# Optimization experiments

Measured on AMD Instinct MI355X. Metric: run time of the kernel, lower is better.

The kernel has to match this reference:

```python
import jax, jax.numpy as jnp
import numpy as np

N_HEAD = 8


def setup_inputs() -> dict:
    key = jax.random.key(0)
    ks = jax.random.split(key, 4)
    B, L, C = 4, 1024, 512
    x = jax.random.normal(ks[0], (B, L, C), dtype=jnp.float32)
    adj = jax.random.uniform(ks[1], (B, L, L), dtype=jnp.float32)
    W_qkv = jax.random.normal(ks[2], (3 * C, C), dtype=jnp.float32) * 0.02
    W_proj = jax.random.normal(ks[3], (C, C), dtype=jnp.float32) * 0.02
    bias_scale = jnp.array([3.0, 3.0], dtype=jnp.float32)
    beta = jnp.ones((3,), dtype=jnp.float32) / 3.0
    return {"x": x, "adj": adj, "W_qkv": W_qkv, "W_proj": W_proj,
            "bias_scale": bias_scale, "beta": beta}


def _branch_attn(Q, K, V, scale, bias=None):
    # Q,K,V: [B,H,L,D]
    S = jnp.einsum('bhqd,bhkd->bhqk', Q, K) / scale
    if bias is not None:
        S = S + bias
    attn = jax.nn.softmax(S, axis=-1)
    return jnp.einsum('bhqk,bhkd->bhqd', attn, V)


def reference(x, adj, W_qkv, W_proj, bias_scale, beta):
    B, L, C = x.shape
    H = N_HEAD
    D = C // H
    scale = jnp.sqrt(jnp.float32(D))

    qkv = x @ W_qkv.T  # [B,L,3C]
    Q, K, V = jnp.split(qkv, 3, axis=-1)
    Q = Q.reshape(B, L, H, D).transpose(0, 2, 1, 3)  # [B,H,L,D]
    K = K.reshape(B, L, H, D).transpose(0, 2, 1, 3)
    V = V.reshape(B, L, H, D).transpose(0, 2, 1, 3)

    # has_cls: zero out CLS row/col in adjacency
    adj_local = adj.at[:, 0, :].set(0.0).at[:, :, 0].set(0.0)
    B_fwd = adj_local[:, None, :, :]              # [B,1,L,L]
    B_bwd = jnp.swapaxes(adj_local, -1, -2)[:, None, :, :]

    h0 = _branch_attn(Q, K, V, scale)
    h1 = _branch_attn(Q, K, V, scale, bias_scale[0] * B_fwd)
    h2 = _branch_attn(Q, K, V, scale, bias_scale[1] * B_bwd)

    b = jax.nn.softmax(beta, axis=0)
    out = b[0] * h0 + b[1] * h1 + b[2] * h2      # [B,H,L,D]
    out = out.transpose(0, 2, 1, 3).reshape(B, L, C)
    return out @ W_proj.T
```

## Files before the change

### kernel.cpp

```cpp
#include <hip/hip_runtime.h>
#include <hip/hip_bf16.h>
#include <stdint.h>

#define B_  4
#define L_  1024
#define C_  512
#define H_  8
#define D_  64
#define BH_ 32
#define M_  4096

typedef short  bf16x8 __attribute__((ext_vector_type(8)));
typedef float  f32x4  __attribute__((ext_vector_type(4)));
typedef unsigned short u16x8 __attribute__((ext_vector_type(8)));
typedef unsigned int   u32x2 __attribute__((ext_vector_type(2)));

__device__ __forceinline__ unsigned short f2bf(float f) {
    union { float f; uint32_t u; } v; v.f = f;
    uint32_t u = v.u;
    return (unsigned short)((u + 0x7fffu + ((u >> 16) & 1u)) >> 16);
}
__device__ __forceinline__ float bf2f(unsigned short s) {
    union { uint32_t u; float f; } v; v.u = ((uint32_t)s) << 16;
    return v.f;
}

__device__ __forceinline__ void gload16(const void* g, void* s) {
    __builtin_amdgcn_global_load_lds((const __attribute__((address_space(1))) void*)g,
                                     (__attribute__((address_space(3))) void*)s, 16, 0, 0);
}

#define NX4   (M_ * C_ / 4)
#define NWQ4  (3 * C_ * C_ / 4)
#define NWP4  (C_ * C_ / 4)
__global__ void cvt_all(const float* __restrict__ x, const float* __restrict__ wq,
                        const float* __restrict__ wp,
                        unsigned short* __restrict__ xb, unsigned short* __restrict__ wqb,
                        unsigned short* __restrict__ wpb) {
    int i = blockIdx.x * 256 + threadIdx.x;
    const float* src; unsigned short* dst; int o;
    if (i < NX4) { src = x; dst = xb; o = i; }
    else if (i < NX4 + NWQ4) { src = wq; dst = wqb; o = i - NX4; }
    else if (i < NX4 + NWQ4 + NWP4) { src = wp; dst = wpb; o = i - NX4 - NWQ4; }
    else return;
    float4 v = ((const float4*)src)[o];
    ushort4 r;
    r.x = f2bf(v.x); r.y = f2bf(v.y); r.z = f2bf(v.z); r.w = f2bf(v.w);
    ((ushort4*)dst)[o] = r;
}

__global__ __launch_bounds__(256) void prep_e(const float* __restrict__ adj,
                                              const float* __restrict__ bias_scale,
                                              unsigned short* __restrict__ EI) {
    __shared__ float Tr[64][65];
    const int b = blockIdx.z, q0 = blockIdx.y * 64, k0 = blockIdx.x * 64;
    const float* adjb = adj + (size_t)b * L_ * L_;
    const int tid = threadIdx.x;
#pragma unroll
    for (int i = 0; i < 4; ++i) {
        int idx = i * 256 + tid;
        int rk = idx >> 4, c4 = (idx & 15) * 4;
        float4 v = *(const float4*)(adjb + (size_t)(k0 + rk) * L_ + q0 + c4);
        Tr[rk][c4 + 0] = v.x; Tr[rk][c4 + 1] = v.y; Tr[rk][c4 + 2] = v.z; Tr[rk][c4 + 3] = v.w;
    }
    __syncthreads();
    const float bs0 = bias_scale[0], bs1 = bias_scale[1];
    const int w = tid >> 6, l = tid & 63, g = l >> 4, c = l & 15;
#pragma unroll
    for (int qs = 0; qs < 4; ++qs) {
        int ql = qs * 16 + c, qg = q0 + ql;
        int klb = w * 16 + g * 4;
        float4 af4 = *(const float4*)(adjb + (size_t)qg * L_ + k0 + klb);
        unsigned short ef[4], eb[4];
        const float afv[4] = {af4.x, af4.y, af4.z, af4.w};
#pragma unroll
        for (int i = 0; i < 4; ++i) {
            int kg = k0 + klb + i;
            bool z = (qg == 0) || (kg == 0);
            ef[i] = f2bf(z ? 1.0f : __expf(bs0 * afv[i]));
            eb[i] = f2bf(z ? 1.0f : __expf(bs1 * Tr[klb + i][ql]));
        }
        size_t o = (((size_t)b * 64 + (blockIdx.y * 4 + qs)) * 64 + (blockIdx.x * 4 + w)) * 512 + (size_t)l * 8;
        u16x8 o8 = {ef[0], ef[1], ef[2], ef[3], eb[0], eb[1], eb[2], eb[3]};
        *(u16x8*)(EI + o) = o8;
    }
}

template <int BM, int BN, int KDIM, int EPI, int NDIM>
__global__ __launch_bounds__(256, 4) void gemm_bf16(const unsigned short* __restrict__ Amat,
                                                    const unsigned short* __restrict__ Bmat,
                                                    float* __restrict__ outp,
                                                    unsigned short* __restrict__ q_out,
                                                    unsigned short* __restrict__ k_out,
                                                    unsigned short* __restrict__ v_out) {
    constexpr int NA = BM / 32, NB = BN / 32;
    constexpr int MI = BM / 32, NI = BN / 32;
    __shared__ __align__(16) unsigned short As[BM * 64];
    __shared__ __align__(16) unsigned short Bs[BN * 64];
    const int tid = threadIdx.x;
    const int l = tid & 63, wid = tid >> 6;
    const int g = l >> 4, c = l & 15;
    const int wr = wid >> 1, wc = wid & 1;
    const int row0 = blockIdx.y * BM, col0 = blockIdx.x * BN;

    f32x4 acc[MI][NI];
#pragma unroll
    for (int mi = 0; mi < MI; ++mi)
#pragma unroll
        for (int ni = 0; ni < NI; ++ni) acc[mi][ni] = (f32x4){0.f, 0.f, 0.f, 0.f};

    for (int k0 = 0; k0 < KDIM; k0 += 64) {
        bf16x8 ra[NA], rb[NB];
#pragma unroll
        for (int i = 0; i < NA; ++i) {
            int q = i * 256 + tid;
            int r = q >> 3, cb = (q & 7) * 16;
            ra[i] = *(const bf16x8*)((const char*)Amat + (size_t)(row0 + r) * (KDIM * 2) + k0 * 2 + cb);
        }
#pragma unroll
        for (int i = 0; i < NB; ++i) {
            int q = i * 256 + tid;
            int r = q >> 3, cb = (q & 7) * 16;
            rb[i] = *(const bf16x8*)((const char*)Bmat + (size_t)(col0 + r) * (KDIM * 2) + k0 * 2 + cb);
        }
        __syncthreads();
#pragma unroll
        for (int i = 0; i < NA; ++i) {
            int q = i * 256 + tid;
            int r = q >> 3, cb = (q & 7) * 16;
            *(bf16x8*)((char*)As + r * 128 + (cb ^ ((r & 7) << 4))) = ra[i];
        }
#pragma unroll
        for (int i = 0; i < NB; ++i) {
            int q = i * 256 + tid;
            int r = q >> 3, cb = (q & 7) * 16;
            *(bf16x8*)((char*)Bs + r * 128 + (cb ^ ((r & 7) << 4))) = rb[i];
        }
        __syncthreads();
#pragma unroll
        for (int kk = 0; kk < 2; ++kk) {
            bf16x8 afr[MI], bfr[NI];
#pragma unroll
            for (int mi = 0; mi < MI; ++mi) {
                int r = wr * (BM / 2) + mi * 16 + c;
                afr[mi] = *(const bf16x8*)((const char*)As + r * 128 + ((kk * 64 + g * 16) ^ ((r & 7) << 4)));
            }
#pragma unroll
            for (int ni = 0; ni < NI; ++ni) {
                int r = wc * (BN / 2) + ni * 16 + c;
                bfr[ni] = *(const bf16x8*)((const char*)Bs + r * 128 + ((kk * 64 + g * 16) ^ ((r & 7) << 4)));
            }
#pragma unroll
            for (int mi = 0; mi < MI; ++mi)
#pragma unroll
                for (int ni = 0; ni < NI; ++ni)
                    acc[mi][ni] = __builtin_amdgcn_mfma_f32_16x16x32_bf16(afr[mi], bfr[ni], acc[mi][ni], 0, 0, 0);
        }
    }
#pragma unroll
    for (int mi = 0; mi < MI; ++mi) {
#pragma unroll
        for (int ni = 0; ni < NI; ++ni) {
#pragma unroll
            for (int ii = 0; ii < 4; ++ii) {
                int m = row0 + wr * (BM / 2) + mi * 16 + g * 4 + ii;
                int n = col0 + wc * (BN / 2) + ni * 16 + c;
                float val = acc[mi][ni][ii];
                if (EPI == 0) {
                    unsigned short v = f2bf(val);
                    int b = m >> 10, ll = m & 1023;
                    int which = n >> 9, cc = n & 511;
                    int hh = cc >> 6, d = cc & 63;
                    int bh = b * 8 + hh;
                    if (which == 0)      q_out[((size_t)bh * L_ + ll) * D_ + d] = v;
                    else if (which == 1) k_out[((size_t)bh * L_ + ll) * D_ + d] = v;
                    else                 v_out[((size_t)bh * D_ + d) * L_ + ll] = v;
                } else {
                    outp[(size_t)m * NDIM + n] = val;
                }
            }
        }
    }
}

struct EReg { bf16x8 e[4]; };

__global__ __launch_bounds__(256, 2) void attn_kernel(const unsigned short* __restrict__ Qb,
                                                      const unsigned short* __restrict__ Kb,
                                                      const unsigned short* __restrict__ Vtb,
                                                      const unsigned short* __restrict__ EI,
                                                      const float* __restrict__ beta,
                                                      unsigned short* __restrict__ hb) {
    __shared__ __align__(16) char smem[2][16384];
    const int tid = threadIdx.x;
    const int w = tid >> 6, l = tid & 63;
    const int g = l >> 4, c = l & 15;

    const int p = blockIdx.x;
    const int s = (p & 7) + 8 * (p >> 6);
    const int h = (p >> 3) & 7;
    const int b = s >> 4, qb = s & 15;
    const int bh = b * 8 + h;
    const int q0 = qb * 64 + w * 16;
    const int qt = qb * 4 + w;

    const unsigned short* Qrow = Qb + ((size_t)bh * L_ + q0 + c) * D_;
    const bf16x8 qf0 = *(const bf16x8*)(Qrow + g * 8);
    const bf16x8 qf1 = *(const bf16x8*)(Qrow + 32 + g * 8);

    const unsigned short* Kbase = Kb + (size_t)bh * L_ * D_;
    const unsigned short* Vbase = Vtb + (size_t)bh * D_ * L_;
    const unsigned short* Ebase = EI + ((size_t)(b * 64 + qt) * 64) * 512;

    f32x4 O[3][4];
#pragma unroll
    for (int j = 0; j < 3; ++j)
#pragma unroll
        for (int dc = 0; dc < 4; ++dc) O[j][dc] = (f32x4){0.f, 0.f, 0.f, 0.f};
    float lsum0 = 0.f, lsum1 = 0.f, lsum2 = 0.f;

    const int srow = l >> 3, sm = l & 7;
    const int key = (c & 7) << 4;

    auto stage = [&](int t, char* base) {
#pragma unroll
        for (int n = 0; n < 2; ++n) {
            int i = 2 * w + n;
            int row = i * 8 + srow;
            int sw = (sm ^ (row & 7)) * 8;
            gload16(Kbase + (size_t)(t * 64 + row) * D_ + sw, base + i * 1024);
            gload16(Vbase + (size_t)row * L_ + t * 64 + sw, base + 8192 + i * 1024);
        }
    };
    auto eload = [&](EReg& X, int t) {
#pragma unroll
        for (int ks = 0; ks < 4; ++ks)
            X.e[ks] = *(const bf16x8*)(Ebase + (size_t)(t * 4 + ks) * 512 + l * 8);
    };

    auto compute = [&](const char* base, const EReg& E) {
        const char* Kl = base;
        const char* Vl = base + 8192;
        unsigned r[4][3][2];
#pragma unroll
        for (int st = 0; st < 4; ++st) {
            const char* kr = Kl + (st * 16 + c) * 128;
            bf16x8 ka = *(const bf16x8*)(kr + ((g * 16) ^ key));
            bf16x8 kb = *(const bf16x8*)(kr + ((64 + g * 16) ^ key));
            f32x4 sacc = (f32x4){0.f, 0.f, 0.f, 0.f};
            sacc = __builtin_amdgcn_mfma_f32_16x16x32_bf16(ka, qf0, sacc, 0, 0, 0);
            sacc = __builtin_amdgcn_mfma_f32_16x16x32_bf16(kb, qf1, sacc, 0, 0, 0);
            float pv[3][4];
#pragma unroll
            for (int i = 0; i < 4; ++i) {
                float p0 = __expf(sacc[i] * 0.125f);
                float p1 = p0 * bf2f((unsigned short)E.e[st][i]);
                float p2 = p0 * bf2f((unsigned short)E.e[st][4 + i]);
                lsum0 += p0; lsum1 += p1; lsum2 += p2;
                pv[0][i] = p0; pv[1][i] = p1; pv[2][i] = p2;
            }
#pragma unroll
            for (int j = 0; j < 3; ++j) {
                r[st][j][0] = __builtin_amdgcn_perm(__float_as_uint(pv[j][1]), __float_as_uint(pv[j][0]), 0x07060302u);
                r[st][j][1] = __builtin_amdgcn_perm(__float_as_uint(pv[j][3]), __float_as_uint(pv[j][2]), 0x07060302u);
            }
        }
#pragma unroll
        for (int kk = 0; kk < 2; ++kk) {
            bf16x8 af[3];
#pragma unroll
            for (int j = 0; j < 3; ++j) {
                union { unsigned u[4]; bf16x8 v; } t_;
                t_.u[0] = r[2 * kk][j][0];     t_.u[1] = r[2 * kk][j][1];
                t_.u[2] = r[2 * kk + 1][j][0]; t_.u[3] = r[2 * kk + 1][j][1];
                af[j] = t_.v;
            }
#pragma unroll
            for (int dc = 0; dc < 4; ++dc) {
                const char* vr = Vl + (dc * 16 + c) * 128;
                u32x2 vlo = *(const u32x2*)(vr + ((kk * 64 + g * 8) ^ key));
                u32x2 vhi = *(const u32x2*)(vr + ((kk * 64 + 32 + g * 8) ^ key));
                union { unsigned u[4]; bf16x8 v; } bv;
                bv.u[0] = vlo[0]; bv.u[1] = vlo[1]; bv.u[2] = vhi[0]; bv.u[3] = vhi[1];
#pragma unroll
                for (int j = 0; j < 3; ++j)
                    O[j][dc] = __builtin_amdgcn_mfma_f32_16x16x32_bf16(af[j], bv.v, O[j][dc], 0, 0, 0);
            }
        }
    };

    EReg E0, E1;
    stage(0, smem[0]);
    eload(E0, 0);
    __syncthreads();
#pragma unroll 1
    for (int t = 0; t < 16; t += 2) {
        stage(t + 1, smem[1]);
        eload(E1, t + 1);
        compute(smem[0], E0);
        __syncthreads();
        if (t + 2 < 16) { stage(t + 2, smem[0]); eload(E0, t + 2); }
        compute(smem[1], E1);
        __syncthreads();
    }

    lsum0 += __shfl_xor(lsum0, 16); lsum0 += __shfl_xor(lsum0, 32);
    lsum1 += __shfl_xor(lsum1, 16); lsum1 += __shfl_xor(lsum1, 32);
    lsum2 += __shfl_xor(lsum2, 16); lsum2 += __shfl_xor(lsum2, 32);

    float b0 = beta[0], b1 = beta[1], b2 = beta[2];
    float bm = fmaxf(b0, fmaxf(b1, b2));
    float e0 = __expf(b0 - bm), e1 = __expf(b1 - bm), e2 = __expf(b2 - bm);
    float inv = 1.0f / (e0 + e1 + e2);
    float i0 = e0 * inv / lsum0, i1 = e1 * inv / lsum1, i2 = e2 * inv / lsum2;

    float iq0[4], iq1[4], iq2[4];
#pragma unroll
    for (int ii = 0; ii < 4; ++ii) {
        iq0[ii] = __shfl(i0, g * 4 + ii);
        iq1[ii] = __shfl(i1, g * 4 + ii);
        iq2[ii] = __shfl(i2, g * 4 + ii);
    }
    const int hcol = (bh & 7) * 64;
#pragma unroll
    for (int dc = 0; dc < 4; ++dc) {
#pragma unroll
        for (int ii = 0; ii < 4; ++ii) {
            float hv = iq0[ii] * O[0][dc][ii] + iq1[ii] * O[1][dc][ii] + iq2[ii] * O[2][dc][ii];
            int qrow = q0 + g * 4 + ii;
            hb[((size_t)(b << 10) + qrow) * C_ + hcol + dc * 16 + c] = f2bf(hv);
        }
    }
}

extern "C" void kernel_launch(void* const* d_in, const int* in_sizes, int n_in,
                              void* d_out, int out_size, void* d_ws, size_t ws_size,
                              hipStream_t stream) {
    const float* x          = (const float*)d_in[0];
    const float* adj        = (const float*)d_in[1];
    const float* wqkv       = (const float*)d_in[2];
    const float* wproj      = (const float*)d_in[3];
    const float* bias_scale = (const float*)d_in[4];
    const float* beta       = (const float*)d_in[5];
    float* out = (float*)d_out;

    char* ws = (char*)d_ws;
    size_t off = 0;
    auto alloc = [&](size_t bytes) {
        void* p = ws + off;
        off += (bytes + 255) & ~(size_t)255;
        return p;
    };
    unsigned short* xb     = (unsigned short*)alloc((size_t)M_ * C_ * 2);
    unsigned short* wqkvb  = (unsigned short*)alloc((size_t)3 * C_ * C_ * 2);
    unsigned short* wprojb = (unsigned short*)alloc((size_t)C_ * C_ * 2);
    unsigned short* Qb     = (unsigned short*)alloc((size_t)BH_ * L_ * D_ * 2);
    unsigned short* Kb     = (unsigned short*)alloc((size_t)BH_ * L_ * D_ * 2);
    unsigned short* Vtb    = (unsigned short*)alloc((size_t)BH_ * D_ * L_ * 2);
    unsigned short* EI     = (unsigned short*)alloc((size_t)B_ * L_ * L_ * 4);
    unsigned short* hb     = (unsigned short*)alloc((size_t)M_ * C_ * 2);

    cvt_all<<<(NX4 + NWQ4 + NWP4 + 255) / 256, 256, 0, stream>>>(x, wqkv, wproj, xb, wqkvb, wprojb);
    prep_e<<<dim3(L_ / 64, L_ / 64, B_), 256, 0, stream>>>(adj, bias_scale, EI);
    gemm_bf16<64, 128, 512, 0, 0><<<dim3(1536 / 128, M_ / 64), 256, 0, stream>>>(xb, wqkvb, nullptr, Qb, Kb, Vtb);
    attn_kernel<<<dim3(512), 256, 0, stream>>>(Qb, Kb, Vtb, EI, beta, hb);
    gemm_bf16<64, 64, 512, 1, 512><<<dim3(512 / 64, M_ / 64), 256, 0, stream>>>(hb, wprojb, out, nullptr, nullptr, nullptr);
}
```

Before: 71.84 us.

## Fuse x conversion into QKV GEMM, symmetric adj tiles, deepen attention pipeline

Removes the separate fp32-to-bf16 conversion of x by converting it inside the QKV GEMM's A-operand load. prep_e now processes tile pairs (i,j) and (j,i) together, so each adjacency tile is read once instead of twice. The attention kernel moves from a two-buffer to a four-buffer LDS pipeline, with explicit vmcnt waits, raw barriers, and S/PV compute split so loads overlap compute further ahead. The four buffers double LDS use to 64KB, which could reduce occupancy, and half of the prep_e blocks now exit immediately.

```diff
diff --git a/kernel.cpp b/kernel.cpp
--- a/kernel.cpp
+++ b/kernel.cpp
@@ -5,7 +5,6 @@
 #define B_  4
 #define L_  1024
 #define C_  512
-#define H_  8
 #define D_  64
 #define BH_ 32
 #define M_  4096
@@ -30,18 +29,14 @@
                                      (__attribute__((address_space(3))) void*)s, 16, 0, 0);
 }
 
-#define NX4   (M_ * C_ / 4)
 #define NWQ4  (3 * C_ * C_ / 4)
 #define NWP4  (C_ * C_ / 4)
-__global__ void cvt_all(const float* __restrict__ x, const float* __restrict__ wq,
-                        const float* __restrict__ wp,
-                        unsigned short* __restrict__ xb, unsigned short* __restrict__ wqb,
-                        unsigned short* __restrict__ wpb) {
+__global__ void cvt_w(const float* __restrict__ wq, const float* __restrict__ wp,
+                      unsigned short* __restrict__ wqb, unsigned short* __restrict__ wpb) {
     int i = blockIdx.x * 256 + threadIdx.x;
     const float* src; unsigned short* dst; int o;
-    if (i < NX4) { src = x; dst = xb; o = i; }
-    else if (i < NX4 + NWQ4) { src = wq; dst = wqb; o = i - NX4; }
-    else if (i < NX4 + NWQ4 + NWP4) { src = wp; dst = wpb; o = i - NX4 - NWQ4; }
+    if (i < NWQ4) { src = wq; dst = wqb; o = i; }
+    else if (i < NWQ4 + NWP4) { src = wp; dst = wpb; o = i - NWQ4; }
     else return;
     float4 v = ((const float4*)src)[o];
     ushort4 r;
@@ -52,42 +47,59 @@
 __global__ __launch_bounds__(256) void prep_e(const float* __restrict__ adj,
                                               const float* __restrict__ bias_scale,
                                               unsigned short* __restrict__ EI) {
-    __shared__ float Tr[64][65];
-    const int b = blockIdx.z, q0 = blockIdx.y * 64, k0 = blockIdx.x * 64;
-    const float* adjb = adj + (size_t)b * L_ * L_;
+    const int bI = blockIdx.z;
+    const int i = blockIdx.y, j = blockIdx.x;
+    if (j < i) return;
+    __shared__ float Ta[64][68];
+    __shared__ float Tb[64][68];
+    const float* adjb = adj + (size_t)bI * L_ * L_;
     const int tid = threadIdx.x;
 #pragma unroll
-    for (int i = 0; i < 4; ++i) {
-        int idx = i * 256 + tid;
-        int rk = idx >> 4, c4 = (idx & 15) * 4;
-        float4 v = *(const float4*)(adjb + (size_t)(k0 + rk) * L_ + q0 + c4);
-        Tr[rk][c4 + 0] = v.x; Tr[rk][c4 + 1] = v.y; Tr[rk][c4 + 2] = v.z; Tr[rk][c4 + 3] = v.w;
+    for (int s = 0; s < 4; ++s) {
+        int idx = s * 256 + tid;
+        int r = idx >> 4, c4 = (idx & 15) * 4;
+        float4 va = *(const float4*)(adjb + (size_t)(i * 64 + r) * L_ + j * 64 + c4);
+        float4 vb = *(const float4*)(adjb + (size_t)(j * 64 + r) * L_ + i * 64 + c4);
+        *(float4*)&Ta[r][c4] = va;
+        *(float4*)&Tb[r][c4] = vb;
     }
     __syncthreads();
     const float bs0 = bias_scale[0], bs1 = bias_scale[1];
     const int w = tid >> 6, l = tid & 63, g = l >> 4, c = l & 15;
+    const int kloc = w * 16 + g * 4;
 #pragma unroll
     for (int qs = 0; qs < 4; ++qs) {
-        int ql = qs * 16 + c, qg = q0 + ql;
-        int klb = w * 16 + g * 4;
-        float4 af4 = *(const float4*)(adjb + (size_t)qg * L_ + k0 + klb);
-        unsigned short ef[4], eb[4];
-        const float afv[4] = {af4.x, af4.y, af4.z, af4.w};
-#pragma unroll
-        for (int i = 0; i < 4; ++i) {
-            int kg = k0 + klb + i;
-            bool z = (qg == 0) || (kg == 0);
-            ef[i] = f2bf(z ? 1.0f : __expf(bs0 * afv[i]));
-            eb[i] = f2bf(z ? 1.0f : __expf(bs1 * Tr[klb + i][ql]));
-        }
-        size_t o = (((size_t)b * 64 + (blockIdx.y * 4 + qs)) * 64 + (blockIdx.x * 4 + w)) * 512 + (size_t)l * 8;
-        u16x8 o8 = {ef[0], ef[1], ef[2], ef[3], eb[0], eb[1], eb[2], eb[3]};
-        *(u16x8*)(EI + o) = o8;
-    }
-}
-
-template <int BM, int BN, int KDIM, int EPI, int NDIM>
+        const int qloc = qs * 16 + c;
+        {
+            int qg = i * 64 + qloc, kgb = j * 64 + kloc;
+            unsigned short ef[4], eb[4];
+#pragma unroll
+            for (int e = 0; e < 4; ++e) {
+                bool z = (qg == 0) || (kgb + e == 0);
+                ef[e] = f2bf(z ? 1.0f : __expf(bs0 * Ta[qloc][kloc + e]));
+                eb[e] = f2bf(z ? 1.0f : __expf(bs1 * Tb[kloc + e][qloc]));
+            }
+            size_t o = (((size_t)bI * 64 + (i * 4 + qs)) * 64 + (j * 4 + w)) * 512 + (size_t)l * 8;
+            *(u16x8*)(EI + o) = (u16x8){ef[0], ef[1], ef[2], ef[3], eb[0], eb[1], eb[2], eb[3]};
+        }
+        if (i != j) {
+            int qg = j * 64 + qloc, kgb = i * 64 + kloc;
+            unsigned short ef[4], eb[4];
+#pragma unroll
+            for (int e = 0; e < 4; ++e) {
+                bool z = (qg == 0) || (kgb + e == 0);
+                ef[e] = f2bf(z ? 1.0f : __expf(bs0 * Tb[qloc][kloc + e]));
+                eb[e] = f2bf(z ? 1.0f : __expf(bs1 * Ta[kloc + e][qloc]));
+            }
+            size_t o = (((size_t)bI * 64 + (j * 4 + qs)) * 64 + (i * 4 + w)) * 512 + (size_t)l * 8;
+            *(u16x8*)(EI + o) = (u16x8){ef[0], ef[1], ef[2], ef[3], eb[0], eb[1], eb[2], eb[3]};
+        }
+    }
+}
+
+template <int BM, int BN, int KDIM, int EPI, int NDIM, bool AF32>
 __global__ __launch_bounds__(256, 4) void gemm_bf16(const unsigned short* __restrict__ Amat,
+                                                    const float* __restrict__ Af,
                                                     const unsigned short* __restrict__ Bmat,
                                                     float* __restrict__ outp,
                                                     unsigned short* __restrict__ q_out,
@@ -114,8 +126,18 @@
 #pragma unroll
         for (int i = 0; i < NA; ++i) {
             int q = i * 256 + tid;
-            int r = q >> 3, cb = (q & 7) * 16;
-            ra[i] = *(const bf16x8*)((const char*)Amat + (size_t)(row0 + r) * (KDIM * 2) + k0 * 2 + cb);
+            int r = q >> 3;
+            if constexpr (AF32) {
+                const float* ap = Af + (size_t)(row0 + r) * KDIM + k0 + (q & 7) * 8;
+                float4 v0 = *(const float4*)ap;
+                float4 v1 = *(const float4*)(ap + 4);
+                union { unsigned short s[8]; bf16x8 v; } u;
+                u.s[0] = f2bf(v0.x); u.s[1] = f2bf(v0.y); u.s[2] = f2bf(v0.z); u.s[3] = f2bf(v0.w);
+                u.s[4] = f2bf(v1.x); u.s[5] = f2bf(v1.y); u.s[6] = f2bf(v1.z); u.s[7] = f2bf(v1.w);
+                ra[i] = u.v;
+            } else {
+                ra[i] = *(const bf16x8*)((const char*)Amat + (size_t)(row0 + r) * (KDIM * 2) + k0 * 2 + (q & 7) * 16);
+            }
         }
 #pragma unroll
         for (int i = 0; i < NB; ++i) {
@@ -191,7 +213,7 @@
                                                       const unsigned short* __restrict__ EI,
                                                       const float* __restrict__ beta,
                                                       unsigned short* __restrict__ hb) {
-    __shared__ __align__(16) char smem[2][16384];
+    __shared__ __align__(16) char smem[4][16384];
     const int tid = threadIdx.x;
     const int w = tid >> 6, l = tid & 63;
     const int g = l >> 4, c = l & 15;
@@ -207,6 +229,7 @@
     const unsigned short* Qrow = Qb + ((size_t)bh * L_ + q0 + c) * D_;
     const bf16x8 qf0 = *(const bf16x8*)(Qrow + g * 8);
     const bf16x8 qf1 = *(const bf16x8*)(Qrow + 32 + g * 8);
+    asm volatile("s_waitcnt vmcnt(0)" ::: "memory");
 
     const unsigned short* Kbase = Kb + (size_t)bh * L_ * D_;
     const unsigned short* Vbase = Vtb + (size_t)bh * D_ * L_;
@@ -238,10 +261,8 @@
             X.e[ks] = *(const bf16x8*)(Ebase + (size_t)(t * 4 + ks) * 512 + l * 8);
     };
 
-    auto compute = [&](const char* base, const EReg& E) {
+    auto computeS = [&](const char* base, const EReg& E, unsigned (&rr)[4][3][2]) {
         const char* Kl = base;
-        const char* Vl = base + 8192;
-        unsigned r[4][3][2];
 #pragma unroll
         for (int st = 0; st < 4; ++st) {
             const char* kr = Kl + (st * 16 + c) * 128;
@@ -261,18 +282,22 @@
             }
 #pragma unroll
             for (int j = 0; j < 3; ++j) {
-                r[st][j][0] = __builtin_amdgcn_perm(__float_as_uint(pv[j][1]), __float_as_uint(pv[j][0]), 0x07060302u);
-                r[st][j][1] = __builtin_amdgcn_perm(__float_as_uint(pv[j][3]), __float_as_uint(pv[j][2]), 0x07060302u);
-            }
-        }
+                rr[st][j][0] = __builtin_amdgcn_perm(__float_as_uint(pv[j][1]), __float_as_uint(pv[j][0]), 0x07060302u);
+                rr[st][j][1] = __builtin_amdgcn_perm(__float_as_uint(pv[j][3]), __float_as_uint(pv[j][2]), 0x07060302u);
+            }
+        }
+    };
+
+    auto computePV = [&](const char* base, const unsigned (&rr)[4][3][2]) {
+        const char* Vl = base + 8192;
 #pragma unroll
         for (int kk = 0; kk < 2; ++kk) {
             bf16x8 af[3];
 #pragma unroll
             for (int j = 0; j < 3; ++j) {
                 union { unsigned u[4]; bf16x8 v; } t_;
-                t_.u[0] = r[2 * kk][j][0];     t_.u[1] = r[2 * kk][j][1];
-                t_.u[2] = r[2 * kk + 1][j][0]; t_.u[3] = r[2 * kk + 1][j][1];
+                t_.u[0] = rr[2 * kk][j][0];     t_.u[1] = rr[2 * kk][j][1];
+                t_.u[2] = rr[2 * kk + 1][j][0]; t_.u[3] = rr[2 * kk + 1][j][1];
                 af[j] = t_.v;
             }
 #pragma unroll
@@ -289,20 +314,46 @@
         }
     };
 
-    EReg E0, E1;
-    stage(0, smem[0]);
-    eload(E0, 0);
-    __syncthreads();
+    EReg EA, EB;
+    stage(0, smem[0]);  asm volatile("" ::: "memory");
+    eload(EA, 0);       asm volatile("" ::: "memory");
+    stage(1, smem[1]);  asm volatile("" ::: "memory");
+    eload(EB, 1);       asm volatile("" ::: "memory");
+
+#define PH_FULL(kk, EX, STT, VMS)                                          \
+    {                                                                      \
+        asm volatile("s_waitcnt vmcnt(" VMS ")" ::: "memory");             \
+        __builtin_amdgcn_s_barrier();                                      \
+        __builtin_amdgcn_sched_barrier(0);                                 \
+        unsigned rr[4][3][2];                                              \
+        stage(STT, smem[(kk + 2) & 3]);  asm volatile("" ::: "memory");    \
+        computeS(smem[kk], EX, rr);                                        \
+        eload(EX, STT);                  asm volatile("" ::: "memory");    \
+        computePV(smem[kk], rr);                                           \
+    }
+#define PH_TAIL(kk, EX, VMS)                                               \
+    {                                                                      \
+        asm volatile("s_waitcnt vmcnt(" VMS ")" ::: "memory");             \
+        __builtin_amdgcn_s_barrier();                                      \
+        __builtin_amdgcn_sched_barrier(0);                                 \
+        unsigned rr[4][3][2];                                              \
+        computeS(smem[kk], EX, rr);                                        \
+        computePV(smem[kk], rr);                                           \
+    }
+
 #pragma unroll 1
-    for (int t = 0; t < 16; t += 2) {
-        stage(t + 1, smem[1]);
-        eload(E1, t + 1);
-        compute(smem[0], E0);
-        __syncthreads();
-        if (t + 2 < 16) { stage(t + 2, smem[0]); eload(E0, t + 2); }
-        compute(smem[1], E1);
-        __syncthreads();
-    }
+    for (int t = 0; t < 12; t += 4) {
+        PH_FULL(0, EA, t + 2, "12")
+        PH_FULL(1, EB, t + 3, "12")
+        PH_FULL(2, EA, t + 4, "12")
+        PH_FULL(3, EB, t + 5, "12")
+    }
+    PH_FULL(0, EA, 14, "12")
+    PH_FULL(1, EB, 15, "12")
+    PH_TAIL(2, EA, "12")
+    PH_TAIL(3, EB, "4")
+#undef PH_FULL
+#undef PH_TAIL
 
     lsum0 += __shfl_xor(lsum0, 16); lsum0 += __shfl_xor(lsum0, 32);
     lsum1 += __shfl_xor(lsum1, 16); lsum1 += __shfl_xor(lsum1, 32);
@@ -351,7 +402,6 @@
         off += (bytes + 255) & ~(size_t)255;
         return p;
     };
-    unsigned short* xb     = (unsigned short*)alloc((size_t)M_ * C_ * 2);
     unsigned short* wqkvb  = (unsigned short*)alloc((size_t)3 * C_ * C_ * 2);
     unsigned short* wprojb = (unsigned short*)alloc((size_t)C_ * C_ * 2);
     unsigned short* Qb     = (unsigned short*)alloc((size_t)BH_ * L_ * D_ * 2);
@@ -360,9 +410,9 @@
     unsigned short* EI     = (unsigned short*)alloc((size_t)B_ * L_ * L_ * 4);
     unsigned short* hb     = (unsigned short*)alloc((size_t)M_ * C_ * 2);
 
-    cvt_all<<<(NX4 + NWQ4 + NWP4 + 255) / 256, 256, 0, stream>>>(x, wqkv, wproj, xb, wqkvb, wprojb);
-    prep_e<<<dim3(L_ / 64, L_ / 64, B_), 256, 0, stream>>>(adj, bias_scale, EI);
-    gemm_bf16<64, 128, 512, 0, 0><<<dim3(1536 / 128, M_ / 64), 256, 0, stream>>>(xb, wqkvb, nullptr, Qb, Kb, Vtb);
+    cvt_w<<<(NWQ4 + NWP4 + 255) / 256, 256, 0, stream>>>(wqkv, wproj, wqkvb, wprojb);
+    prep_e<<<dim3(16, 16, B_), 256, 0, stream>>>(adj, bias_scale, EI);
+    gemm_bf16<64, 128, 512, 0, 0, true><<<dim3(1536 / 128, M_ / 64), 256, 0, stream>>>(nullptr, x, wqkvb, nullptr, Qb, Kb, Vtb);
     attn_kernel<<<dim3(512), 256, 0, stream>>>(Qb, Kb, Vtb, EI, beta, hb);
-    gemm_bf16<64, 64, 512, 1, 512><<<dim3(512 / 64, M_ / 64), 256, 0, stream>>>(hb, wprojb, out, nullptr, nullptr, nullptr);
-}
+    gemm_bf16<64, 64, 512, 1, 512, false><<<dim3(512 / 64, M_ / 64), 256, 0, stream>>>(hb, nullptr, wprojb, out, nullptr, nullptr, nullptr);
+}
```

New measurement: 113.6 us. 1.58x slower.
